# Optimization experiments

Hardware: AMD Instinct MI355X
Metric: run time of the kernel (lower is better)

## Reference

```python
import jax, jax.numpy as jnp
import numpy as np
from jax import lax

B, CIN, H, W = 4, 64, 256, 256
Q, K = 256, 16


def _conv3x3_replicate(x, w, b):
    # replicate (edge) padding of 1, then VALID conv -> same spatial size
    xp = jnp.pad(x, ((0, 0), (0, 0), (1, 1), (1, 1)), mode='edge')
    y = lax.conv_general_dilated(xp, w, (1, 1), 'VALID',
                                 dimension_numbers=('NCHW', 'OIHW', 'NCHW'))
    return y + b[None, :, None, None]


def setup_inputs() -> dict:
    key = jax.random.key(0)
    ks = jax.random.split(key, 9)
    s1 = 1.0 / np.sqrt(CIN * 9)
    s2 = 1.0 / np.sqrt(Q * 9)
    s3 = 1.0 / np.sqrt(Q)
    return {
        'x':  jax.random.normal(ks[0], (B, CIN, H, W), jnp.float32),
        'w1': jax.random.normal(ks[1], (Q, CIN, 3, 3), jnp.float32) * s1,
        'b1': jax.random.normal(ks[2], (Q,), jnp.float32) * s1,
        'w2': jax.random.normal(ks[3], (Q, Q, 3, 3), jnp.float32) * s2,
        'b2': jax.random.normal(ks[4], (Q,), jnp.float32) * s2,
        'w3': jax.random.normal(ks[5], (Q, Q, 1, 1), jnp.float32) * s3,
        'b3': jax.random.normal(ks[6], (Q,), jnp.float32) * s3,
        'mu': jax.random.normal(ks[7], (K, Q), jnp.float32),      # cluster_mu squeezed
        'label': jax.random.normal(ks[8], (K,), jnp.float32),
    }


def reference(x, w1, b1, w2, b2, w3, b3, mu, label):
    # query_encoder: Convx2 (conv3x3 replicate + relu, twice) then 1x1 conv
    q = jax.nn.relu(_conv3x3_replicate(x, w1, b1))
    q = jax.nn.relu(_conv3x3_replicate(q, w2, b2))
    q = jnp.einsum('oc,bchw->bohw', w3[:, :, 0, 0], q) + b3[None, :, None, None]
    # logit[b,k,h,w] = -sum_c (q - mu)^2, via norm expansion (no BxKxCxHxW tensor)
    q2 = jnp.sum(q * q, axis=1, keepdims=True)                   # (B,1,H,W)
    mu2 = jnp.sum(mu * mu, axis=1)                               # (K,)
    cross = jnp.einsum('bchw,kc->bkhw', q, mu)                   # (B,K,H,W)
    logit = -(q2 - 2.0 * cross + mu2[None, :, None, None])
    att = jax.nn.softmax(logit, axis=1)                          # softmax over clusters
    out = jnp.einsum('bkhw,k->bhw', att, label)
    return out[:, None]                                          # (B,1,H,W)
```

## Files before the change

kernel.cpp:

```cpp
#include <hip/hip_runtime.h>

#define BB   4
#define CIN  64
#define HH   256
#define WW   256
#define QQ   256
#define KK   16

typedef _Float16 half8 __attribute__((ext_vector_type(8)));
typedef float   f32x16 __attribute__((ext_vector_type(16)));
typedef unsigned int u32;

#define OFF_W1R   0ull
#define OFF_W2R   294912ull
#define OFF_WMU   1474560ull
#define OFF_LGB   1490944ull
#define OFF_ACT0  1605888ull
#define OFF_ACT1  35160320ull

__device__ __forceinline__ void dma16(const void* g, void* l) {
  __builtin_amdgcn_global_load_lds(
      (const __attribute__((address_space(1))) u32*)g,
      (__attribute__((address_space(3))) u32*)l, 16, 0, 0);
}

__global__ __launch_bounds__(256) void k_prep(
    const float* __restrict__ w1, const float* __restrict__ w2,
    const float* __restrict__ w3, const float* __restrict__ b3,
    const float* __restrict__ mu,
    _Float16* __restrict__ w1r, _Float16* __restrict__ w2r,
    float* __restrict__ wpart, float* __restrict__ lgb) {
  int bid = blockIdx.x, tid = threadIdx.x;
  if (bid < 576) {
    int idx = bid * 256 + tid;
    int blk = idx >> 13;
    int cc = blk / 9, tt = blk - cc * 9;
    int rem = idx & 8191;
    int n = rem >> 5, r = rem & 31;
    int q = (r >> 3) ^ ((n >> 1) & 3), e = r & 7;
    int c = cc * 32 + q * 8 + e;
    w1r[idx] = (_Float16)w1[(n * 64 + c) * 9 + tt];
  } else if (bid < 2880) {
    int d = (bid - 576) * 256 + tid;
    int blk = d >> 13;
    int cc = blk / 9, tt = blk - cc * 9;
    int rem = d & 8191;
    int n = rem >> 5, r = rem & 31;
    int q = (r >> 3) ^ ((n >> 1) & 3), e = r & 7;
    int c = cc * 32 + q * 8 + e;
    w2r[d] = (_Float16)w2[(n * 256 + c) * 9 + tt];
  } else if (bid < 3008) {
    int j = bid - 2880;
    int k = j >> 3, o0 = (j & 7) << 5;
    float s = 0.f;
#pragma unroll 4
    for (int oi = 0; oi < 32; ++oi) {
      int o = o0 + oi;
      s = fmaf(mu[k * 256 + o], w3[o * 256 + tid], s);
    }
    wpart[j * 256 + tid] = s;
  } else {
    int k = bid - 3008;
    float m = mu[k * 256 + tid];
    __shared__ float red[256];
    red[tid] = m * (2.f * b3[tid] - m);
    __syncthreads();
    for (int st = 128; st > 0; st >>= 1) {
      if (tid < st) red[tid] += red[tid + st];
      __syncthreads();
    }
    if (tid == 0) lgb[k] = red[0];
  }
}

__global__ __launch_bounds__(256) void k_prep2(
    const float* __restrict__ wpart, float* __restrict__ wmu2) {
  int k = blockIdx.x, tid = threadIdx.x;
  float s = 0.f;
#pragma unroll
  for (int p = 0; p < 8; ++p) s += wpart[(k * 8 + p) * 256 + tid];
  wmu2[k * 256 + tid] = 2.f * s;
}

__global__ __launch_bounds__(256) void k_t0(const float* __restrict__ x,
                                            _Float16* __restrict__ act0) {
  __shared__ float tile[64][65];
  int blk = blockIdx.x;
  int b = blk >> 10;
  int p0 = (blk & 1023) << 6;
  int t = threadIdx.x;
  {
    int p = t & 63, c0 = t >> 6;
    const float* xb = x + (size_t)b * (CIN * 65536) + p0 + p;
#pragma unroll
    for (int i = 0; i < 16; ++i) {
      int c = c0 + (i << 2);
      tile[c][p] = xb[(size_t)c * 65536];
    }
  }
  __syncthreads();
  {
    _Float16* o = act0 + (size_t)(b * 65536 + p0) * CIN;
#pragma unroll
    for (int uu = 0; uu < 2; ++uu) {
      int u = t + (uu << 8);
      int px = u & 63, oct = u >> 6;
      half8 h;
#pragma unroll
      for (int i = 0; i < 8; ++i) h[i] = (_Float16)tile[oct * 8 + i][px];
      *(half8*)(o + px * CIN + oct * 8) = h;
    }
  }
}

template <int CI>
__global__ __launch_bounds__(256, 2) void k_conv(
    const _Float16* __restrict__ actin, const char* __restrict__ wr,
    const float* __restrict__ bias, _Float16* __restrict__ actout) {
  constexpr int NC = CI / 32;
  constexpr int NT = 9 * NC;
  __shared__ __align__(16) char smem[67584];
  auto As = (char(*)[12288])smem;
  auto Bs = (char(*)[16384])(smem + 24576);
  _Float16* Qs = (_Float16*)smem;

  int tid = threadIdx.x;
  int b = blockIdx.x >> 9;
  int tile = blockIdx.x & 511;
  int txi = tile & 15, tyi = tile >> 4;
  int x0 = txi << 4, y0 = tyi << 3;
  int lane = tid & 63, wave = tid >> 6;
  int mwave = wave >> 1, nwave = wave & 1;
  int l31 = lane & 31, khalf = lane >> 5;

  f32x16 acc[2][4];
#pragma unroll
  for (int s = 0; s < 2; ++s)
#pragma unroll
    for (int nt = 0; nt < 4; ++nt)
#pragma unroll
      for (int r = 0; r < 16; ++r) acc[s][nt][r] = 0.f;

  const char* aG[3];
  int aL[3];
#pragma unroll
  for (int i = 0; i < 3; ++i) {
    int px = (wave * 3 + i) * 16 + (lane >> 2);
    int s = lane & 3;
    int pxc = min(px, 179);
    int hy = pxc / 18, hx = pxc - hy * 18;
    int y = min(max(y0 - 1 + hy, 0), 255);
    int x = min(max(x0 - 1 + hx, 0), 255);
    int q = s ^ ((pxc >> 1) & 3);
    aG[i] = (const char*)actin +
            (((size_t)(b * 65536 + y * 256 + x)) * CI + q * 8) * 2;
    aL[i] = (wave * 3 + i) * 1024;
  }
  const char* bG = wr + wave * 4096 + lane * 16;
  int bL = wave * 4096;

#pragma unroll
  for (int i = 0; i < 3; ++i) dma16(aG[i], &As[0][aL[i]]);
#pragma unroll
  for (int i = 0; i < 4; ++i) dma16(bG + i * 1024, &Bs[0][bL + i * 1024]);
  __syncthreads();

  for (int cc = 0; cc < NC; ++cc) {
#pragma unroll
    for (int t = 0; t < 9; ++t) {
      int j = cc * 9 + t;
      if (j + 1 < NT) {
        const char* bsrc = bG + (size_t)(j + 1) * 16384;
        char* bdst = &Bs[(j + 1) & 1][bL];
#pragma unroll
        for (int i = 0; i < 4; ++i) dma16(bsrc + i * 1024, bdst + i * 1024);
        if (t == 8) {
#pragma unroll
          for (int i = 0; i < 3; ++i)
            dma16(aG[i] + (cc + 1) * 64, &As[(cc + 1) & 1][aL[i]]);
        }
      }
      int dy = t / 3, dx = t - dy * 3;
      const char* Ab = As[cc & 1];
      const char* Bb = Bs[j & 1];
      half8 af[2][2], bf[2][4];
#pragma unroll
      for (int s = 0; s < 2; ++s) {
        int px = (mwave * 4 + s * 2 + (l31 >> 4) + dy) * 18 + (l31 & 15) + dx;
        int sw = ((px >> 1) & 3) << 4;
#pragma unroll
        for (int ks = 0; ks < 2; ++ks) {
          int q = (ks * 2 + khalf) << 4;
          af[ks][s] = *(const half8*)(Ab + px * 64 + (q ^ sw));
        }
      }
#pragma unroll
      for (int nt = 0; nt < 4; ++nt) {
        int n = nwave * 128 + nt * 32 + l31;
        int sw = ((n >> 1) & 3) << 4;
#pragma unroll
        for (int ks = 0; ks < 2; ++ks) {
          int q = (ks * 2 + khalf) << 4;
          bf[ks][nt] = *(const half8*)(Bb + n * 64 + (q ^ sw));
        }
      }
#pragma unroll
      for (int ks = 0; ks < 2; ++ks)
#pragma unroll
        for (int s = 0; s < 2; ++s)
#pragma unroll
          for (int nt = 0; nt < 4; ++nt)
            acc[s][nt] = __builtin_amdgcn_mfma_f32_32x32x16_f16(
                af[ks][s], bf[ks][nt], acc[s][nt], 0, 0, 0);
      __syncthreads();
    }
  }

#pragma unroll
  for (int s = 0; s < 2; ++s)
#pragma unroll
    for (int nt = 0; nt < 4; ++nt) {
      int n = nwave * 128 + nt * 32 + l31;
      float bn = bias[n];
#pragma unroll
      for (int r = 0; r < 16; ++r) {
        int mrow = (r & 3) + 8 * (r >> 2) + 4 * khalf;
        int p = (mwave * 4 + s * 2 + (mrow >> 4)) * 16 + (mrow & 15);
        Qs[p * 264 + n] = (_Float16)fmaxf(acc[s][nt][r] + bn, 0.f);
      }
    }
  __syncthreads();
  {
    _Float16* gout = actout + (((size_t)(b * 65536 + y0 * 256 + x0)) << 8);
#pragma unroll
    for (int i = 0; i < 16; ++i) {
      int f = tid + (i << 8);
      int p = f >> 5, o = f & 31;
      half8 v = *(const half8*)&Qs[p * 264 + o * 8];
      *(half8*)(gout + (((p >> 4) * 256 + (p & 15)) << 8) + o * 8) = v;
    }
  }
}

__global__ __launch_bounds__(256) void k_head(
    const _Float16* __restrict__ a2_0, const _Float16* __restrict__ a2_1,
    const _Float16* __restrict__ a2_2, const _Float16* __restrict__ a2_3,
    const float* __restrict__ wmu2, const float* __restrict__ lgb,
    const float* __restrict__ label, float* __restrict__ out) {
  int b = blockIdx.x >> 8;
  int px = (blockIdx.x & 255) * 256 + threadIdx.x;
  const _Float16* base = (b == 0) ? a2_0 : (b == 1) ? a2_1
                       : (b == 2) ? a2_2 : a2_3;
  const half8* ap = (const half8*)(base + ((size_t)px << 8));
  float cr[16];
#pragma unroll
  for (int k = 0; k < 16; ++k) cr[k] = lgb[k];
#pragma unroll 2
  for (int cc = 0; cc < 32; ++cc) {
    half8 h = ap[cc];
    float a0 = (float)h[0], a1 = (float)h[1], a2 = (float)h[2],
          a3 = (float)h[3], a4 = (float)h[4], a5 = (float)h[5],
          a6 = (float)h[6], a7 = (float)h[7];
#pragma unroll
    for (int k = 0; k < 16; ++k) {
      const float* w = wmu2 + (k << 8) + (cc << 3);
      float c0 = cr[k];
      c0 = fmaf(a0, w[0], c0);
      c0 = fmaf(a1, w[1], c0);
      c0 = fmaf(a2, w[2], c0);
      c0 = fmaf(a3, w[3], c0);
      c0 = fmaf(a4, w[4], c0);
      c0 = fmaf(a5, w[5], c0);
      c0 = fmaf(a6, w[6], c0);
      c0 = fmaf(a7, w[7], c0);
      cr[k] = c0;
    }
  }
  float mx = cr[0];
#pragma unroll
  for (int k = 1; k < 16; ++k) mx = fmaxf(mx, cr[k]);
  float num = 0.f, den = 0.f;
#pragma unroll
  for (int k = 0; k < 16; ++k) {
    float e = __expf(cr[k] - mx);
    num = fmaf(e, label[k], num);
    den += e;
  }
  out[(size_t)b * 65536 + px] = num / den;
}

extern "C" void kernel_launch(void* const* d_in, const int* in_sizes, int n_in,
                              void* d_out, int out_size, void* d_ws, size_t ws_size,
                              hipStream_t stream) {
  const float* x  = (const float*)d_in[0];
  const float* w1 = (const float*)d_in[1];
  const float* b1 = (const float*)d_in[2];
  const float* w2 = (const float*)d_in[3];
  const float* b2 = (const float*)d_in[4];
  const float* w3 = (const float*)d_in[5];
  const float* b3 = (const float*)d_in[6];
  const float* mu = (const float*)d_in[7];
  const float* label = (const float*)d_in[8];
  float* out = (float*)d_out;

  char* ws = (char*)d_ws;
  _Float16* w1r  = (_Float16*)(ws + OFF_W1R);
  _Float16* w2r  = (_Float16*)(ws + OFF_W2R);
  float*    wmu2 = (float*)   (ws + OFF_WMU);
  float*    lgb  = (float*)   (ws + OFF_LGB);
  _Float16* act0 = (_Float16*)(ws + OFF_ACT0);
  _Float16* act1 = (_Float16*)(ws + OFF_ACT1);
  float*    wpart = (float*)  (ws + OFF_ACT1);

  _Float16* a2d[4] = {
    (_Float16*)(ws + OFF_ACT0),
    act1 + 0 * (size_t)65536 * 256,
    act1 + 1 * (size_t)65536 * 256,
    act1 + 2 * (size_t)65536 * 256
  };

  k_prep<<<3024, 256, 0, stream>>>(w1, w2, w3, b3, mu, w1r, w2r, wpart, lgb);
  k_prep2<<<16, 256, 0, stream>>>(wpart, wmu2);
  k_t0<<<4096, 256, 0, stream>>>(x, act0);
  k_conv<64><<<2048, 256, 0, stream>>>(act0, (const char*)w1r, b1, act1);
  for (int b = 0; b < BB; ++b)
    k_conv<256><<<512, 256, 0, stream>>>(act1 + (size_t)b * 65536 * 256,
                                         (const char*)w2r, b2, a2d[b]);
  k_head<<<1024, 256, 0, stream>>>(a2d[0], a2d[1], a2d[2], a2d[3],
                                   wmu2, lgb, label, out);
}
```

Baseline: 593.2 us.

## Load conv weights directly into registers and cut per-tap barriers

The weight repack now uses an MFMA-fragment-friendly layout. The conv kernel loads B fragments straight from global memory into double-buffered registers instead of staging them through LDS. Activation tiles are still DMA'd to LDS, but barriers drop from one per 3x3 tap to one per channel chunk, with explicit vmcnt waits and setprio around the MFMAs. The aim is to remove LDS traffic and barrier stalls for the weights. In exchange it raises register pressure and relies on L2 and L1 to serve the weights shared across blocks.

```diff
diff --git a/kernel.cpp b/kernel.cpp
--- a/kernel.cpp
+++ b/kernel.cpp
@@ -36,18 +36,22 @@
     int blk = idx >> 13;
     int cc = blk / 9, tt = blk - cc * 9;
     int rem = idx & 8191;
-    int n = rem >> 5, r = rem & 31;
-    int q = (r >> 3) ^ ((n >> 1) & 3), e = r & 7;
-    int c = cc * 32 + q * 8 + e;
+    int ks = rem >> 12;
+    int n  = (rem >> 4) & 255;
+    int kh = (rem >> 3) & 1;
+    int e  = rem & 7;
+    int c = cc * 32 + ks * 16 + kh * 8 + e;
     w1r[idx] = (_Float16)w1[(n * 64 + c) * 9 + tt];
   } else if (bid < 2880) {
     int d = (bid - 576) * 256 + tid;
     int blk = d >> 13;
     int cc = blk / 9, tt = blk - cc * 9;
     int rem = d & 8191;
-    int n = rem >> 5, r = rem & 31;
-    int q = (r >> 3) ^ ((n >> 1) & 3), e = r & 7;
-    int c = cc * 32 + q * 8 + e;
+    int ks = rem >> 12;
+    int n  = (rem >> 4) & 255;
+    int kh = (rem >> 3) & 1;
+    int e  = rem & 7;
+    int c = cc * 32 + ks * 16 + kh * 8 + e;
     w2r[d] = (_Float16)w2[(n * 256 + c) * 9 + tt];
   } else if (bid < 3008) {
     int j = bid - 2880;
@@ -121,7 +125,6 @@
   constexpr int NT = 9 * NC;
   __shared__ __align__(16) char smem[67584];
   auto As = (char(*)[12288])smem;
-  auto Bs = (char(*)[16384])(smem + 24576);
   _Float16* Qs = (_Float16*)smem;
 
   int tid = threadIdx.x;
@@ -156,34 +159,51 @@
             (((size_t)(b * 65536 + y * 256 + x)) * CI + q * 8) * 2;
     aL[i] = (wave * 3 + i) * 1024;
   }
-  const char* bG = wr + wave * 4096 + lane * 16;
-  int bL = wave * 4096;
+
+  const char* b0 = wr + ((nwave * 128 + l31) * 32 + khalf * 16);
+  const char* b1 = b0 + 8192;
 
 #pragma unroll
   for (int i = 0; i < 3; ++i) dma16(aG[i], &As[0][aL[i]]);
-#pragma unroll
-  for (int i = 0; i < 4; ++i) dma16(bG + i * 1024, &Bs[0][bL + i * 1024]);
-  __syncthreads();
-
-  for (int cc = 0; cc < NC; ++cc) {
-#pragma unroll
-    for (int t = 0; t < 9; ++t) {
-      int j = cc * 9 + t;
-      if (j + 1 < NT) {
-        const char* bsrc = bG + (size_t)(j + 1) * 16384;
-        char* bdst = &Bs[(j + 1) & 1][bL];
-#pragma unroll
-        for (int i = 0; i < 4; ++i) dma16(bsrc + i * 1024, bdst + i * 1024);
-        if (t == 8) {
-#pragma unroll
-          for (int i = 0; i < 3; ++i)
-            dma16(aG[i] + (cc + 1) * 64, &As[(cc + 1) & 1][aL[i]]);
+
+  half8 bf[2][2][4];
+#pragma unroll
+  for (int nt = 0; nt < 4; ++nt) {
+    bf[0][0][nt] = *(const half8*)(b0 + nt * 1024);
+    bf[0][1][nt] = *(const half8*)(b1 + nt * 1024);
+  }
+  b0 += 16384; b1 += 16384;
+  asm volatile("s_waitcnt vmcnt(8)" ::: "memory");
+  __builtin_amdgcn_s_barrier();
+
+  for (int c2 = 0; c2 < NC; c2 += 2) {
+    bool last2 = (c2 + 2 >= NC);
+#pragma unroll
+    for (int u = 0; u < 18; ++u) {
+      int t = (u < 9) ? u : u - 9;
+      constexpr int dummy = 0; (void)dummy;
+      int pr = u & 1;
+      if (u == 6) {
+#pragma unroll
+        for (int i = 0; i < 3; ++i)
+          dma16(aG[i] + (c2 + 1) * 64, &As[1][aL[i]]);
+      }
+      if (u == 15 && !last2) {
+#pragma unroll
+        for (int i = 0; i < 3; ++i)
+          dma16(aG[i] + (c2 + 2) * 64, &As[0][aL[i]]);
+      }
+      if (!(last2 && u == 17)) {
+#pragma unroll
+        for (int nt = 0; nt < 4; ++nt) {
+          bf[pr ^ 1][0][nt] = *(const half8*)(b0 + nt * 1024);
+          bf[pr ^ 1][1][nt] = *(const half8*)(b1 + nt * 1024);
         }
-      }
+        b0 += 16384; b1 += 16384;
+      }
+      const char* Ab = As[(u >= 9) ? 1 : 0];
       int dy = t / 3, dx = t - dy * 3;
-      const char* Ab = As[cc & 1];
-      const char* Bb = Bs[j & 1];
-      half8 af[2][2], bf[2][4];
+      half8 af[2][2];
 #pragma unroll
       for (int s = 0; s < 2; ++s) {
         int px = (mwave * 4 + s * 2 + (l31 >> 4) + dy) * 18 + (l31 & 15) + dx;
@@ -194,16 +214,7 @@
           af[ks][s] = *(const half8*)(Ab + px * 64 + (q ^ sw));
         }
       }
-#pragma unroll
-      for (int nt = 0; nt < 4; ++nt) {
-        int n = nwave * 128 + nt * 32 + l31;
-        int sw = ((n >> 1) & 3) << 4;
-#pragma unroll
-        for (int ks = 0; ks < 2; ++ks) {
-          int q = (ks * 2 + khalf) << 4;
-          bf[ks][nt] = *(const half8*)(Bb + n * 64 + (q ^ sw));
-        }
-      }
+      __builtin_amdgcn_s_setprio(1);
 #pragma unroll
       for (int ks = 0; ks < 2; ++ks)
 #pragma unroll
@@ -211,10 +222,19 @@
 #pragma unroll
           for (int nt = 0; nt < 4; ++nt)
             acc[s][nt] = __builtin_amdgcn_mfma_f32_32x32x16_f16(
-                af[ks][s], bf[ks][nt], acc[s][nt], 0, 0, 0);
-      __syncthreads();
-    }
-  }
+                af[ks][s], bf[pr][ks][nt], acc[s][nt], 0, 0, 0);
+      __builtin_amdgcn_s_setprio(0);
+      if (u == 8) {
+        asm volatile("s_waitcnt vmcnt(8) lgkmcnt(0)" ::: "memory");
+        __builtin_amdgcn_s_barrier();
+      }
+      if (u == 17 && !last2) {
+        asm volatile("s_waitcnt vmcnt(8) lgkmcnt(0)" ::: "memory");
+        __builtin_amdgcn_s_barrier();
+      }
+    }
+  }
+  __syncthreads();
 
 #pragma unroll
   for (int s = 0; s < 2; ++s)
```

New measurement: 612.8 us. 1.03x slower.
